# Kernel optimization log

Hardware: AMD Instinct MI355X
Metric: run time of the kernel (lower is better)

## Reference

```python
import jax, jax.numpy as jnp
import numpy as np

N_NODES = 30000
N_EDGES = 480000
N_GRAPHS = 64
NEG_SLOPE = 0.2


def gat_layer(h, src, dst, W, a_l, a_r, b):
    # h: [N, F_in], W: [F_in, H*D], a_l/a_r: [H, D], b: [H*D]
    N = h.shape[0]
    H, D = a_l.shape
    feat = (h @ W).reshape(N, H, D)
    el = jnp.sum(feat * a_l[None], axis=-1)  # [N, H]
    er = jnp.sum(feat * a_r[None], axis=-1)  # [N, H]
    e = jax.nn.leaky_relu(el[src] + er[dst], NEG_SLOPE)  # [E, H]
    # edge-softmax over incoming edges of each dst node (numerically stable)
    emax = jax.ops.segment_max(e, dst, num_segments=N)          # [N, H]
    ex = jnp.exp(e - emax[dst])                                  # [E, H]
    denom = jax.ops.segment_sum(ex, dst, num_segments=N)        # [N, H]
    alpha = ex / denom[dst]                                      # [E, H]
    msg = feat[src] * alpha[..., None]                           # [E, H, D]
    out = jax.ops.segment_sum(msg, dst, num_segments=N)         # [N, H, D]
    return out.reshape(N, H * D) + b


def setup_inputs() -> dict:
    key = jax.random.key(0)
    ks = jax.random.split(key, 16)
    feat = jax.random.normal(ks[0], (N_NODES, 6), dtype=jnp.float32)
    src = jax.random.randint(ks[1], (N_EDGES,), 0, N_NODES)
    dst = jax.random.randint(ks[2], (N_EDGES,), 0, N_NODES)
    graph_id = jnp.sort(jax.random.randint(ks[3], (N_NODES,), 0, N_GRAPHS))
    s = 0.1
    W1 = jax.random.normal(ks[4], (6, 128), dtype=jnp.float32) * s
    al1 = jax.random.normal(ks[5], (4, 32), dtype=jnp.float32) * s
    ar1 = jax.random.normal(ks[6], (4, 32), dtype=jnp.float32) * s
    b1 = jnp.zeros((128,), dtype=jnp.float32)
    W2 = jax.random.normal(ks[7], (128, 128), dtype=jnp.float32) * s
    al2 = jax.random.normal(ks[8], (4, 32), dtype=jnp.float32) * s
    ar2 = jax.random.normal(ks[9], (4, 32), dtype=jnp.float32) * s
    b2 = jnp.zeros((128,), dtype=jnp.float32)
    W3 = jax.random.normal(ks[10], (128, 256), dtype=jnp.float32) * s
    al3 = jax.random.normal(ks[11], (4, 64), dtype=jnp.float32) * s
    ar3 = jax.random.normal(ks[12], (4, 64), dtype=jnp.float32) * s
    b3 = jnp.zeros((256,), dtype=jnp.float32)
    return {"feat": feat, "src": src, "dst": dst, "graph_id": graph_id,
            "W1": W1, "al1": al1, "ar1": ar1, "b1": b1,
            "W2": W2, "al2": al2, "ar2": ar2, "b2": b2,
            "W3": W3, "al3": al3, "ar3": ar3, "b3": b3}


def reference(feat, src, dst, graph_id, W1, al1, ar1, b1, W2, al2, ar2, b2, W3, al3, ar3, b3):
    h = gat_layer(feat, src, dst, W1, al1, ar1, b1)  # [N, 128]
    h = jax.nn.relu(h)                                # dropout is identity in eval
    h = gat_layer(h, src, dst, W2, al2, ar2, b2)      # [N, 128]
    h = jax.nn.relu(h)
    h = gat_layer(h, src, dst, W3, al3, ar3, b3)      # [N, 256]
    # dgl.mean_nodes over batched graphs
    hs = jax.ops.segment_sum(h, graph_id, num_segments=N_GRAPHS)  # [G, 256]
    cnt = jax.ops.segment_sum(jnp.ones((h.shape[0],), h.dtype), graph_id, num_segments=N_GRAPHS)
    hg = hs / jnp.maximum(cnt, 1.0)[:, None]
    return hg
```

## Files before the change

kernel.cpp:

```cpp
#include <hip/hip_runtime.h>

typedef _Float16 h4 __attribute__((ext_vector_type(4)));
typedef _Float16 h8v __attribute__((ext_vector_type(8)));
typedef float f4v __attribute__((ext_vector_type(4)));
typedef float f32x8 __attribute__((ext_vector_type(8)));


__global__ void zero_i32(int* __restrict__ p, int n) {
    int i = blockIdx.x * blockDim.x + threadIdx.x;
    if (i < n) p[i] = 0;
}

__global__ void hist_kernel(const int* __restrict__ dst, int* __restrict__ counts, int E) {
    int i = blockIdx.x * blockDim.x + threadIdx.x;
    if (i < E) atomicAdd(&counts[dst[i]], 1);
}

__global__ void scan_block(const int* __restrict__ counts, int* __restrict__ rowptr,
                           int* __restrict__ bsum, int n) {
    __shared__ int wsum[16];
    const int tid = threadIdx.x;
    const int lane = tid & 63, wv = tid >> 6;
    const int i = blockIdx.x * 1024 + tid;
    int v = (i < n) ? counts[i] : 0;
    int x = v;
#pragma unroll
    for (int off = 1; off < 64; off <<= 1) {
        int t = __shfl_up(x, off);
        if (lane >= off) x += t;
    }
    if (lane == 63) wsum[wv] = x;
    __syncthreads();
    if (tid < 16) {
        int y = wsum[tid];
#pragma unroll
        for (int off = 1; off < 16; off <<= 1) {
            int t = __shfl_up(y, off);
            if (tid >= off) y += t;
        }
        wsum[tid] = y;
    }
    __syncthreads();
    int woff = (wv > 0) ? wsum[wv - 1] : 0;
    if (i < n) rowptr[i] = woff + x - v;
    if (tid == 0) bsum[blockIdx.x] = wsum[15];
}

__global__ void scan_tops(int* __restrict__ bsum, int* __restrict__ rowptr, int nb, int n) {
    const int tid = threadIdx.x;
    int v = (tid < nb) ? bsum[tid] : 0;
    int x = v;
#pragma unroll
    for (int off = 1; off < 64; off <<= 1) {
        int t = __shfl_up(x, off);
        if (tid >= off) x += t;
    }
    if (tid < nb) bsum[tid] = x - v;
    if (tid == 63) rowptr[n] = x;
}

__global__ void scan_add(int* __restrict__ rowptr, const int* __restrict__ bsum, int n) {
    int b = blockIdx.x;
    int i = b * 1024 + threadIdx.x;
    if (i < n && b > 0) rowptr[i] += bsum[b];
}

__global__ void scatter_kernel(const int* __restrict__ src, const int* __restrict__ dst,
                               const int* __restrict__ rowptr, int* __restrict__ cursor,
                               int* __restrict__ srcs, int E) {
    int i = blockIdx.x * blockDim.x + threadIdx.x;
    if (i < E) {
        int d = dst[i];
        int p = rowptr[d] + atomicAdd(&cursor[d], 1);
        srcs[p] = src[i];
    }
}

template <int K, int FOUT>
__global__ void pack_w(const float* __restrict__ W, _Float16* __restrict__ Wp) {
    constexpr int KS = K / 32;
    constexpr int CT = FOUT / 16;
    int idx = blockIdx.x * blockDim.x + threadIdx.x;
    if (idx >= CT * KS * 64) return;
    int l = idx & 63;
    int ks = (idx >> 6) % KS;
    int ct = idx / (64 * KS);
    int kbase = ks * 32 + (l >> 4) * 8;
    int col = ct * 16 + (l & 15);
    h8v v;
#pragma unroll
    for (int e = 0; e < 8; e++) v[e] = (_Float16)W[(size_t)(kbase + e) * FOUT + col];
    *reinterpret_cast<h8v*>(&Wp[(size_t)idx * 8]) = v;
}

template <int FIN, int FOUT, int D, bool RELU_IN>
__global__ void gemm_att(const float* __restrict__ A, const float* __restrict__ bin,
                         const float* __restrict__ W, const float* __restrict__ al,
                         const float* __restrict__ ar, _Float16* __restrict__ feat,
                         float* __restrict__ el, float* __restrict__ er, int N) {
    constexpr int R = 16;
    constexpr int H = FOUT / D;
    constexpr int T = FOUT / 2;
    __shared__ __align__(16) float As[FIN][R + 4];
    const int j = threadIdx.x;
    const int h0 = j / D;
    const int h1 = (j + T) / D;
    const float alv0 = al[j],     arv0 = ar[j];
    const float alv1 = al[j + T], arv1 = ar[j + T];
    const int row0 = blockIdx.x * R;

    for (int idx = threadIdx.x; idx < R * FIN; idx += T) {
        int r = idx / FIN, k = idx % FIN;
        int rr = row0 + r;
        float v = 0.f;
        if (rr < N) {
            v = A[(size_t)rr * FIN + k];
            if constexpr (RELU_IN) { v += bin[k]; v = fmaxf(v, 0.f); }
        }
        As[k][r] = v;
    }
    __syncthreads();

    float acc0[R], acc1[R];
#pragma unroll
    for (int r = 0; r < R; r++) { acc0[r] = 0.f; acc1[r] = 0.f; }

    for (int k = 0; k < FIN; k++) {
        float w0 = W[(size_t)k * FOUT + j];
        float w1 = W[(size_t)k * FOUT + j + T];
        const float4* ap = reinterpret_cast<const float4*>(&As[k][0]);
        float av[16];
        *reinterpret_cast<float4*>(&av[0])  = ap[0];
        *reinterpret_cast<float4*>(&av[4])  = ap[1];
        *reinterpret_cast<float4*>(&av[8])  = ap[2];
        *reinterpret_cast<float4*>(&av[12]) = ap[3];
#pragma unroll
        for (int r = 0; r < R; r++) {
            acc0[r] += av[r] * w0;
            acc1[r] += av[r] * w1;
        }
    }

#pragma unroll
    for (int r = 0; r < R; r++) {
        int rr = row0 + r;
        if (rr >= N) break;
        float v0 = acc0[r], v1 = acc1[r];
        feat[(size_t)rr * FOUT + j] = (_Float16)v0;
        feat[(size_t)rr * FOUT + j + T] = (_Float16)v1;
        float vl0 = v0 * alv0, vr0 = v0 * arv0;
        float vl1 = v1 * alv1, vr1 = v1 * arv1;
#pragma unroll
        for (int off = D / 2; off >= 1; off >>= 1) {
            vl0 += __shfl_xor(vl0, off);
            vr0 += __shfl_xor(vr0, off);
            vl1 += __shfl_xor(vl1, off);
            vr1 += __shfl_xor(vr1, off);
        }
        if ((j % D) == 0) {
            el[(size_t)rr * H + h0] = vl0;
            er[(size_t)rr * H + h0] = vr0;
            el[(size_t)rr * H + h1] = vl1;
            er[(size_t)rr * H + h1] = vr1;
        }
    }
}

template <int K, int FOUT, int D, bool RELU_IN>
__global__ __launch_bounds__(256)
void gemm_mfma(const float* __restrict__ A, const float* __restrict__ bin,
               const _Float16* __restrict__ Wp, const float* __restrict__ al,
               const float* __restrict__ ar, _Float16* __restrict__ feat,
               float* __restrict__ el, float* __restrict__ er, int N) {
    constexpr int RB  = 32;
    constexpr int KS  = K / 32;
    constexpr int CHW = FOUT / 2;
    constexpr int CTW = CHW / 16;
    constexpr int CTH = D / 16;
    constexpr int HW  = CTW / CTH;
    constexpr int H   = FOUT / D;
    constexpr int STR = K + 8;
    __shared__ _Float16 As[RB * STR];
    const int tid = threadIdx.x;
    const int w  = tid >> 6;
    const int l  = tid & 63;
    const int rt = w >> 1;
    const int ch = w & 1;
    const int row0 = blockIdx.x * RB;

    constexpr int NV4 = RB * K / 4;
    for (int v = tid; v < NV4; v += 256) {
        int r  = v / (K / 4);
        int kv = (v % (K / 4)) * 4;
        int rr = row0 + r;
        float4 x = {0.f, 0.f, 0.f, 0.f};
        if (rr < N) {
            x = *reinterpret_cast<const float4*>(&A[(size_t)rr * K + kv]);
            if constexpr (RELU_IN) {
                float4 bv = *reinterpret_cast<const float4*>(&bin[kv]);
                x.x = fmaxf(x.x + bv.x, 0.f);
                x.y = fmaxf(x.y + bv.y, 0.f);
                x.z = fmaxf(x.z + bv.z, 0.f);
                x.w = fmaxf(x.w + bv.w, 0.f);
            }
        }
        h4 hv;
        hv[0] = (_Float16)x.x; hv[1] = (_Float16)x.y;
        hv[2] = (_Float16)x.z; hv[3] = (_Float16)x.w;
        *reinterpret_cast<h4*>(&As[r * STR + kv]) = hv;
    }
    __syncthreads();

    h8v afrag[KS];
    {
        const _Float16* base = &As[(rt * 16 + (l & 15)) * STR + ((l >> 4) * 8)];
#pragma unroll
        for (int ks = 0; ks < KS; ks++)
            afrag[ks] = *reinterpret_cast<const h8v*>(&base[ks * 32]);
    }

    const h8v* Wv = reinterpret_cast<const h8v*>(Wp);
    const int ct0 = ch * CTW;
    f4v acc[CTW];
#pragma unroll
    for (int c = 0; c < CTW; c++) acc[c] = (f4v){0.f, 0.f, 0.f, 0.f};

    h8v bfr[2][KS];
#pragma unroll
    for (int ks = 0; ks < KS; ks++) bfr[0][ks] = Wv[(size_t)((ct0 * KS + ks) * 64 + l)];
#pragma unroll
    for (int c = 0; c < CTW; c++) {
        const int cur = c & 1, nxt = cur ^ 1;
        if (c + 1 < CTW) {
#pragma unroll
            for (int ks = 0; ks < KS; ks++)
                bfr[nxt][ks] = Wv[(size_t)(((ct0 + c + 1) * KS + ks) * 64 + l)];
        }
#pragma unroll
        for (int ks = 0; ks < KS; ks++)
            acc[c] = __builtin_amdgcn_mfma_f32_16x16x32_f16(afrag[ks], bfr[cur][ks], acc[c], 0, 0, 0);
    }

    float elp[HW][4], erp[HW][4];
#pragma unroll
    for (int hh = 0; hh < HW; hh++)
#pragma unroll
        for (int r = 0; r < 4; r++) { elp[hh][r] = 0.f; erp[hh][r] = 0.f; }

#pragma unroll
    for (int c = 0; c < CTW; c++) {
        const int col = ch * CHW + c * 16 + (l & 15);
        const float alv = al[col], arv = ar[col];
        const int hh = c / CTH;
#pragma unroll
        for (int r = 0; r < 4; r++) {
            float v = acc[c][r];
            elp[hh][r] += v * alv;
            erp[hh][r] += v * arv;
            int rr = row0 + rt * 16 + (l >> 4) * 4 + r;
            if (rr < N) feat[(size_t)rr * FOUT + col] = (_Float16)v;
        }
    }
#pragma unroll
    for (int hh = 0; hh < HW; hh++) {
#pragma unroll
        for (int r = 0; r < 4; r++) {
            float v = elp[hh][r], u = erp[hh][r];
#pragma unroll
            for (int off = 8; off >= 1; off >>= 1) {
                v += __shfl_xor(v, off);
                u += __shfl_xor(u, off);
            }
            if ((l & 15) == 0) {
                int rr = row0 + rt * 16 + (l >> 4) * 4 + r;
                if (rr < N) {
                    int hg = ch * HW + hh;
                    el[(size_t)rr * H + hg] = v;
                    er[(size_t)rr * H + hg] = u;
                }
            }
        }
    }
}

template <int HD, int D>
__global__ __launch_bounds__(256)
void agg_fused(const h8v* __restrict__ featH8, const float* __restrict__ el,
               const float* __restrict__ er, const int* __restrict__ srcs,
               const int* __restrict__ rowptr, f32x8* __restrict__ out, int N) {
    constexpr int TPN = HD / 8;
    constexpr int NPB = 256 / TPN;
    const int tid = threadIdx.x;
    const int ln = tid % TPN;
    const int node = blockIdx.x * NPB + tid / TPN;
    if (node >= N) return;
    const int h = ln / (D / 8);
    const int beg = rowptr[node], end = rowptr[node + 1];
    const float ern = er[(size_t)node * 4 + h];

    float s = 0.f;
    f32x8 a0 = {0,0,0,0,0,0,0,0}, a1 = a0;
    int i = beg;
    for (; i + 4 <= end; i += 4) {
        int u0 = srcs[i], u1 = srcs[i + 1], u2 = srcs[i + 2], u3 = srcs[i + 3];
        float x0 = el[(size_t)u0 * 4 + h] + ern; x0 = x0 > 0.f ? x0 : 0.2f * x0;
        float x1 = el[(size_t)u1 * 4 + h] + ern; x1 = x1 > 0.f ? x1 : 0.2f * x1;
        float x2 = el[(size_t)u2 * 4 + h] + ern; x2 = x2 > 0.f ? x2 : 0.2f * x2;
        float x3 = el[(size_t)u3 * 4 + h] + ern; x3 = x3 > 0.f ? x3 : 0.2f * x3;
        h8v f0 = featH8[(size_t)u0 * TPN + ln];
        h8v f1 = featH8[(size_t)u1 * TPN + ln];
        h8v f2 = featH8[(size_t)u2 * TPN + ln];
        h8v f3 = featH8[(size_t)u3 * TPN + ln];
        float w0 = __expf(x0), w1 = __expf(x1);
        float w2 = __expf(x2), w3 = __expf(x3);
        s += (w0 + w1) + (w2 + w3);
#pragma unroll
        for (int k = 0; k < 8; k++) {
            a0[k] += w0 * (float)f0[k];
            a1[k] += w1 * (float)f1[k];
            a0[k] += w2 * (float)f2[k];
            a1[k] += w3 * (float)f3[k];
        }
    }
    for (; i < end; i++) {
        int u = srcs[i];
        float x = el[(size_t)u * 4 + h] + ern; x = x > 0.f ? x : 0.2f * x;
        h8v f = featH8[(size_t)u * TPN + ln];
        float w = __expf(x);
        s += w;
#pragma unroll
        for (int k = 0; k < 8; k++) a0[k] += w * (float)f[k];
    }
    const float inv = (s > 0.f) ? 1.f / s : 0.f;
    f32x8 o;
#pragma unroll
    for (int k = 0; k < 8; k++) o[k] = (a0[k] + a1[k]) * inv;
    out[(size_t)node * TPN + ln] = o;
}


__device__ __forceinline__ int lower_bound_i(const int* __restrict__ a, int n, int key) {
    int lo = 0, hi = n;
    while (lo < hi) {
        int mid = (lo + hi) >> 1;
        if (a[mid] < key) lo = mid + 1; else hi = mid;
    }
    return lo;
}

__global__ void readout_partial(const float* __restrict__ agg, const int* __restrict__ gid,
                                float* __restrict__ part, int N, int C, int SL) {
    int g = blockIdx.x / SL, slice = blockIdx.x % SL;
    int c = threadIdx.x;
    int start = lower_bound_i(gid, N, g);
    int end = lower_bound_i(gid, N, g + 1);
    float sum = 0.f;
    for (int n = start + slice; n < end; n += SL) sum += agg[(size_t)n * C + c];
    part[((size_t)g * SL + slice) * C + c] = sum;
}

__global__ void readout_final(const float* __restrict__ part, const float* __restrict__ b3,
                              const int* __restrict__ gid, float* __restrict__ out,
                              int N, int C, int SL) {
    int g = blockIdx.x, c = threadIdx.x;
    int start = lower_bound_i(gid, N, g);
    int end = lower_bound_i(gid, N, g + 1);
    int cnt = end - start;
    float s = 0.f;
    for (int k = 0; k < SL; k++) s += part[((size_t)g * SL + k) * C + c];
    out[(size_t)g * C + c] = (cnt > 0) ? s / (float)cnt + b3[c] : 0.f;
}


extern "C" void kernel_launch(void* const* d_in, const int* in_sizes, int n_in,
                              void* d_out, int out_size, void* d_ws, size_t ws_size,
                              hipStream_t stream) {
    const float* feat0 = (const float*)d_in[0];
    const int* src = (const int*)d_in[1];
    const int* dst = (const int*)d_in[2];
    const int* gid = (const int*)d_in[3];
    const float* W1 = (const float*)d_in[4];
    const float* al1 = (const float*)d_in[5];
    const float* ar1 = (const float*)d_in[6];
    const float* b1 = (const float*)d_in[7];
    const float* W2 = (const float*)d_in[8];
    const float* al2 = (const float*)d_in[9];
    const float* ar2 = (const float*)d_in[10];
    const float* b2 = (const float*)d_in[11];
    const float* W3 = (const float*)d_in[12];
    const float* al3 = (const float*)d_in[13];
    const float* ar3 = (const float*)d_in[14];
    const float* b3 = (const float*)d_in[15];

    const int N = in_sizes[0] / 6;
    const int E = in_sizes[1];
    const int G = 64;
    const int SL = 8;
    float* out = (float*)d_out;

    char* wsp = (char*)d_ws;
    auto alloc = [&](size_t bytes) -> char* {
        char* p = wsp;
        wsp += (bytes + 255) & ~(size_t)255;
        return p;
    };
    int* counts   = (int*)alloc((size_t)N * 4);
    int* rowptr   = (int*)alloc((size_t)(N + 1) * 4);
    int* cursor   = (int*)alloc((size_t)N * 4);
    int* bsum     = (int*)alloc(64 * 4);
    int* srcs     = (int*)alloc((size_t)E * 4);
    float* el     = (float*)alloc((size_t)N * 4 * 4);
    float* er     = (float*)alloc((size_t)N * 4 * 4);
    _Float16* featH = (_Float16*)alloc((size_t)N * 256 * 2);
    float* aggB   = (float*)alloc((size_t)N * 256 * 4);
    float* part   = (float*)alloc((size_t)G * SL * 256 * 4);
    _Float16* Wp2 = (_Float16*)alloc((size_t)128 * 128 * 2);
    _Float16* Wp3 = (_Float16*)alloc((size_t)128 * 256 * 2);

    const int nb = (N + 1023) / 1024;
    const int zspan = (int)(((char*)bsum - (char*)counts) / 4) + 64;
    zero_i32<<<dim3((zspan + 255) / 256), dim3(256), 0, stream>>>(counts, zspan);
    hist_kernel<<<dim3((E + 255) / 256), dim3(256), 0, stream>>>(dst, counts, E);
    scan_block<<<dim3(nb), dim3(1024), 0, stream>>>(counts, rowptr, bsum, N);
    scan_tops<<<dim3(1), dim3(64), 0, stream>>>(bsum, rowptr, nb, N);
    scan_add<<<dim3(nb), dim3(1024), 0, stream>>>(rowptr, bsum, N);
    scatter_kernel<<<dim3((E + 255) / 256), dim3(256), 0, stream>>>(
        src, dst, rowptr, cursor, srcs, E);

    pack_w<128, 128><<<dim3(8), dim3(256), 0, stream>>>(W2, Wp2);
    pack_w<128, 256><<<dim3(16), dim3(256), 0, stream>>>(W3, Wp3);

    gemm_att<6, 128, 32, false><<<dim3((N + 15) / 16), dim3(64), 0, stream>>>(
        feat0, nullptr, W1, al1, ar1, featH, el, er, N);
    agg_fused<128, 32><<<dim3((N + 15) / 16), dim3(256), 0, stream>>>(
        (const h8v*)featH, el, er, srcs, rowptr, (f32x8*)aggB, N);

    gemm_mfma<128, 128, 32, true><<<dim3((N + 31) / 32), dim3(256), 0, stream>>>(
        aggB, b1, Wp2, al2, ar2, featH, el, er, N);
    agg_fused<128, 32><<<dim3((N + 15) / 16), dim3(256), 0, stream>>>(
        (const h8v*)featH, el, er, srcs, rowptr, (f32x8*)aggB, N);

    gemm_mfma<128, 256, 64, true><<<dim3((N + 31) / 32), dim3(256), 0, stream>>>(
        aggB, b2, Wp3, al3, ar3, featH, el, er, N);
    agg_fused<256, 64><<<dim3((N + 7) / 8), dim3(256), 0, stream>>>(
        (const h8v*)featH, el, er, srcs, rowptr, (f32x8*)aggB, N);

    readout_partial<<<dim3(G * SL), dim3(256), 0, stream>>>(aggB, gid, part, N, 256, SL);
    readout_final<<<dim3(G), dim3(256), 0, stream>>>(part, b3, gid, out, N, 256, SL);
}
```

Before: 213.5 us.

## Fuse bias+ReLU into aggregation epilogue with fp16 output, merge small launches

New measurement: 209.9 us. About the same (-1.7%).

```diff
diff --git a/kernel.cpp b/kernel.cpp
--- a/kernel.cpp
+++ b/kernel.cpp
@@ -46,23 +46,26 @@
     if (tid == 0) bsum[blockIdx.x] = wsum[15];
 }
 
-__global__ void scan_tops(int* __restrict__ bsum, int* __restrict__ rowptr, int nb, int n) {
+__global__ void scan_add_tops(int* __restrict__ rowptr, const int* __restrict__ bsum,
+                              int nb, int n) {
+    __shared__ int off_s, tot_s;
+    const int b = blockIdx.x;
     const int tid = threadIdx.x;
-    int v = (tid < nb) ? bsum[tid] : 0;
-    int x = v;
-#pragma unroll
-    for (int off = 1; off < 64; off <<= 1) {
-        int t = __shfl_up(x, off);
-        if (tid >= off) x += t;
-    }
-    if (tid < nb) bsum[tid] = x - v;
-    if (tid == 63) rowptr[n] = x;
-}
-
-__global__ void scan_add(int* __restrict__ rowptr, const int* __restrict__ bsum, int n) {
-    int b = blockIdx.x;
-    int i = b * 1024 + threadIdx.x;
-    if (i < n && b > 0) rowptr[i] += bsum[b];
+    if (tid < 64) {
+        int v = (tid < nb) ? bsum[tid] : 0;
+        int x = v;
+#pragma unroll
+        for (int off = 1; off < 64; off <<= 1) {
+            int t = __shfl_up(x, off);
+            if (tid >= off) x += t;
+        }
+        if (tid == 63) tot_s = x;
+        if (tid == b) off_s = x - v;
+    }
+    __syncthreads();
+    int i = b * 1024 + tid;
+    if (i < n) rowptr[i] += off_s;
+    if (b == 0 && tid == 0) rowptr[n] = tot_s;
 }
 
 __global__ void scatter_kernel(const int* __restrict__ src, const int* __restrict__ dst,
@@ -76,15 +79,19 @@
     }
 }
 
-template <int K, int FOUT>
-__global__ void pack_w(const float* __restrict__ W, _Float16* __restrict__ Wp) {
-    constexpr int KS = K / 32;
-    constexpr int CT = FOUT / 16;
+__global__ void pack_w_both(const float* __restrict__ W2, _Float16* __restrict__ Wp2,
+                            const float* __restrict__ W3, _Float16* __restrict__ Wp3) {
     int idx = blockIdx.x * blockDim.x + threadIdx.x;
-    if (idx >= CT * KS * 64) return;
+    const float* W; _Float16* Wp; int FOUT;
+    if (idx < 2048) { W = W2; Wp = Wp2; FOUT = 128; }
+    else {
+        idx -= 2048;
+        if (idx >= 4096) return;
+        W = W3; Wp = Wp3; FOUT = 256;
+    }
     int l = idx & 63;
-    int ks = (idx >> 6) % KS;
-    int ct = idx / (64 * KS);
+    int ks = (idx >> 6) & 3;
+    int ct = idx >> 8;
     int kbase = ks * 32 + (l >> 4) * 8;
     int col = ct * 16 + (l & 15);
     h8v v;
@@ -93,11 +100,11 @@
     *reinterpret_cast<h8v*>(&Wp[(size_t)idx * 8]) = v;
 }
 
-template <int FIN, int FOUT, int D, bool RELU_IN>
-__global__ void gemm_att(const float* __restrict__ A, const float* __restrict__ bin,
-                         const float* __restrict__ W, const float* __restrict__ al,
-                         const float* __restrict__ ar, _Float16* __restrict__ feat,
-                         float* __restrict__ el, float* __restrict__ er, int N) {
+template <int FIN, int FOUT, int D>
+__global__ void gemm_att(const float* __restrict__ A, const float* __restrict__ W,
+                         const float* __restrict__ al, const float* __restrict__ ar,
+                         _Float16* __restrict__ feat, float* __restrict__ el,
+                         float* __restrict__ er, int N) {
     constexpr int R = 16;
     constexpr int H = FOUT / D;
     constexpr int T = FOUT / 2;
@@ -112,12 +119,7 @@
     for (int idx = threadIdx.x; idx < R * FIN; idx += T) {
         int r = idx / FIN, k = idx % FIN;
         int rr = row0 + r;
-        float v = 0.f;
-        if (rr < N) {
-            v = A[(size_t)rr * FIN + k];
-            if constexpr (RELU_IN) { v += bin[k]; v = fmaxf(v, 0.f); }
-        }
-        As[k][r] = v;
+        As[k][r] = (rr < N) ? A[(size_t)rr * FIN + k] : 0.f;
     }
     __syncthreads();
 
@@ -166,12 +168,12 @@
     }
 }
 
-template <int K, int FOUT, int D, bool RELU_IN>
+template <int K, int FOUT, int D>
 __global__ __launch_bounds__(256)
-void gemm_mfma(const float* __restrict__ A, const float* __restrict__ bin,
-               const _Float16* __restrict__ Wp, const float* __restrict__ al,
-               const float* __restrict__ ar, _Float16* __restrict__ feat,
-               float* __restrict__ el, float* __restrict__ er, int N) {
+void gemm_mfma(const _Float16* __restrict__ A, const _Float16* __restrict__ Wp,
+               const float* __restrict__ al, const float* __restrict__ ar,
+               _Float16* __restrict__ feat, float* __restrict__ el,
+               float* __restrict__ er, int N) {
     constexpr int RB  = 32;
     constexpr int KS  = K / 32;
     constexpr int CHW = FOUT / 2;
@@ -188,26 +190,14 @@
     const int ch = w & 1;
     const int row0 = blockIdx.x * RB;
 
-    constexpr int NV4 = RB * K / 4;
-    for (int v = tid; v < NV4; v += 256) {
-        int r  = v / (K / 4);
-        int kv = (v % (K / 4)) * 4;
+    constexpr int NV8 = RB * K / 8;
+    for (int v = tid; v < NV8; v += 256) {
+        int r  = v / (K / 8);
+        int kv = (v % (K / 8)) * 8;
         int rr = row0 + r;
-        float4 x = {0.f, 0.f, 0.f, 0.f};
-        if (rr < N) {
-            x = *reinterpret_cast<const float4*>(&A[(size_t)rr * K + kv]);
-            if constexpr (RELU_IN) {
-                float4 bv = *reinterpret_cast<const float4*>(&bin[kv]);
-                x.x = fmaxf(x.x + bv.x, 0.f);
-                x.y = fmaxf(x.y + bv.y, 0.f);
-                x.z = fmaxf(x.z + bv.z, 0.f);
-                x.w = fmaxf(x.w + bv.w, 0.f);
-            }
-        }
-        h4 hv;
-        hv[0] = (_Float16)x.x; hv[1] = (_Float16)x.y;
-        hv[2] = (_Float16)x.z; hv[3] = (_Float16)x.w;
-        *reinterpret_cast<h4*>(&As[r * STR + kv]) = hv;
+        h8v x = {};
+        if (rr < N) x = *reinterpret_cast<const h8v*>(&A[(size_t)rr * K + kv]);
+        *reinterpret_cast<h8v*>(&As[r * STR + kv]) = x;
     }
     __syncthreads();
 
@@ -283,11 +273,12 @@
     }
 }
 
-template <int HD, int D>
+template <int HD, int D, bool FP16OUT>
 __global__ __launch_bounds__(256)
 void agg_fused(const h8v* __restrict__ featH8, const float* __restrict__ el,
                const float* __restrict__ er, const int* __restrict__ srcs,
-               const int* __restrict__ rowptr, f32x8* __restrict__ out, int N) {
+               const int* __restrict__ rowptr, const float* __restrict__ bias,
+               void* __restrict__ outp, int N) {
     constexpr int TPN = HD / 8;
     constexpr int NPB = 256 / TPN;
     const int tid = threadIdx.x;
@@ -300,17 +291,29 @@
 
     float s = 0.f;
     f32x8 a0 = {0,0,0,0,0,0,0,0}, a1 = a0;
+
     int i = beg;
+    int alend = (beg + 3) & ~3;
+    if (alend > end) alend = end;
+    for (; i < alend; i++) {
+        int u = srcs[i];
+        float x = el[(size_t)u * 4 + h] + ern; x = x > 0.f ? x : 0.2f * x;
+        h8v f = featH8[(size_t)u * TPN + ln];
+        float w = __expf(x);
+        s += w;
+#pragma unroll
+        for (int k = 0; k < 8; k++) a0[k] += w * (float)f[k];
+    }
     for (; i + 4 <= end; i += 4) {
-        int u0 = srcs[i], u1 = srcs[i + 1], u2 = srcs[i + 2], u3 = srcs[i + 3];
-        float x0 = el[(size_t)u0 * 4 + h] + ern; x0 = x0 > 0.f ? x0 : 0.2f * x0;
-        float x1 = el[(size_t)u1 * 4 + h] + ern; x1 = x1 > 0.f ? x1 : 0.2f * x1;
-        float x2 = el[(size_t)u2 * 4 + h] + ern; x2 = x2 > 0.f ? x2 : 0.2f * x2;
-        float x3 = el[(size_t)u3 * 4 + h] + ern; x3 = x3 > 0.f ? x3 : 0.2f * x3;
-        h8v f0 = featH8[(size_t)u0 * TPN + ln];
-        h8v f1 = featH8[(size_t)u1 * TPN + ln];
-        h8v f2 = featH8[(size_t)u2 * TPN + ln];
-        h8v f3 = featH8[(size_t)u3 * TPN + ln];
+        int4 uu = *reinterpret_cast<const int4*>(&srcs[i]);
+        float x0 = el[(size_t)uu.x * 4 + h] + ern; x0 = x0 > 0.f ? x0 : 0.2f * x0;
+        float x1 = el[(size_t)uu.y * 4 + h] + ern; x1 = x1 > 0.f ? x1 : 0.2f * x1;
+        float x2 = el[(size_t)uu.z * 4 + h] + ern; x2 = x2 > 0.f ? x2 : 0.2f * x2;
+        float x3 = el[(size_t)uu.w * 4 + h] + ern; x3 = x3 > 0.f ? x3 : 0.2f * x3;
+        h8v f0 = featH8[(size_t)uu.x * TPN + ln];
+        h8v f1 = featH8[(size_t)uu.y * TPN + ln];
+        h8v f2 = featH8[(size_t)uu.z * TPN + ln];
+        h8v f3 = featH8[(size_t)uu.w * TPN + ln];
         float w0 = __expf(x0), w1 = __expf(x1);
         float w2 = __expf(x2), w3 = __expf(x3);
         s += (w0 + w1) + (w2 + w3);
@@ -332,10 +335,21 @@
         for (int k = 0; k < 8; k++) a0[k] += w * (float)f[k];
     }
     const float inv = (s > 0.f) ? 1.f / s : 0.f;
-    f32x8 o;
-#pragma unroll
-    for (int k = 0; k < 8; k++) o[k] = (a0[k] + a1[k]) * inv;
-    out[(size_t)node * TPN + ln] = o;
+    if constexpr (FP16OUT) {
+        const float4 b0 = *reinterpret_cast<const float4*>(&bias[ln * 8]);
+        const float4 b1v = *reinterpret_cast<const float4*>(&bias[ln * 8 + 4]);
+        float bb[8] = {b0.x, b0.y, b0.z, b0.w, b1v.x, b1v.y, b1v.z, b1v.w};
+        h8v o;
+#pragma unroll
+        for (int k = 0; k < 8; k++)
+            o[k] = (_Float16)fmaxf((a0[k] + a1[k]) * inv + bb[k], 0.f);
+        reinterpret_cast<h8v*>(outp)[(size_t)node * TPN + ln] = o;
+    } else {
+        f32x8 o;
+#pragma unroll
+        for (int k = 0; k < 8; k++) o[k] = (a0[k] + a1[k]) * inv;
+        reinterpret_cast<f32x8*>(outp)[(size_t)node * TPN + ln] = o;
+    }
 }
 
 
@@ -412,6 +426,7 @@
     float* el     = (float*)alloc((size_t)N * 4 * 4);
     float* er     = (float*)alloc((size_t)N * 4 * 4);
     _Float16* featH = (_Float16*)alloc((size_t)N * 256 * 2);
+    _Float16* aggH  = (_Float16*)alloc((size_t)N * 128 * 2);
     float* aggB   = (float*)alloc((size_t)N * 256 * 4);
     float* part   = (float*)alloc((size_t)G * SL * 256 * 4);
     _Float16* Wp2 = (_Float16*)alloc((size_t)128 * 128 * 2);
@@ -422,28 +437,26 @@
     zero_i32<<<dim3((zspan + 255) / 256), dim3(256), 0, stream>>>(counts, zspan);
     hist_kernel<<<dim3((E + 255) / 256), dim3(256), 0, stream>>>(dst, counts, E);
     scan_block<<<dim3(nb), dim3(1024), 0, stream>>>(counts, rowptr, bsum, N);
-    scan_tops<<<dim3(1), dim3(64), 0, stream>>>(bsum, rowptr, nb, N);
-    scan_add<<<dim3(nb), dim3(1024), 0, stream>>>(rowptr, bsum, N);
+    scan_add_tops<<<dim3(nb), dim3(1024), 0, stream>>>(rowptr, bsum, nb, N);
     scatter_kernel<<<dim3((E + 255) / 256), dim3(256), 0, stream>>>(
         src, dst, rowptr, cursor, srcs, E);
 
-    pack_w<128, 128><<<dim3(8), dim3(256), 0, stream>>>(W2, Wp2);
-    pack_w<128, 256><<<dim3(16), dim3(256), 0, stream>>>(W3, Wp3);
-
-    gemm_att<6, 128, 32, false><<<dim3((N + 15) / 16), dim3(64), 0, stream>>>(
-        feat0, nullptr, W1, al1, ar1, featH, el, er, N);
-    agg_fused<128, 32><<<dim3((N + 15) / 16), dim3(256), 0, stream>>>(
-        (const h8v*)featH, el, er, srcs, rowptr, (f32x8*)aggB, N);
-
-    gemm_mfma<128, 128, 32, true><<<dim3((N + 31) / 32), dim3(256), 0, stream>>>(
-        aggB, b1, Wp2, al2, ar2, featH, el, er, N);
-    agg_fused<128, 32><<<dim3((N + 15) / 16), dim3(256), 0, stream>>>(
-        (const h8v*)featH, el, er, srcs, rowptr, (f32x8*)aggB, N);
-
-    gemm_mfma<128, 256, 64, true><<<dim3((N + 31) / 32), dim3(256), 0, stream>>>(
-        aggB, b2, Wp3, al3, ar3, featH, el, er, N);
-    agg_fused<256, 64><<<dim3((N + 7) / 8), dim3(256), 0, stream>>>(
-        (const h8v*)featH, el, er, srcs, rowptr, (f32x8*)aggB, N);
+    pack_w_both<<<dim3(24), dim3(256), 0, stream>>>(W2, Wp2, W3, Wp3);
+
+    gemm_att<6, 128, 32><<<dim3((N + 15) / 16), dim3(64), 0, stream>>>(
+        feat0, W1, al1, ar1, featH, el, er, N);
+    agg_fused<128, 32, true><<<dim3((N + 15) / 16), dim3(256), 0, stream>>>(
+        (const h8v*)featH, el, er, srcs, rowptr, b1, aggH, N);
+
+    gemm_mfma<128, 128, 32><<<dim3((N + 31) / 32), dim3(256), 0, stream>>>(
+        aggH, Wp2, al2, ar2, featH, el, er, N);
+    agg_fused<128, 32, true><<<dim3((N + 15) / 16), dim3(256), 0, stream>>>(
+        (const h8v*)featH, el, er, srcs, rowptr, b2, aggH, N);
+
+    gemm_mfma<128, 256, 64><<<dim3((N + 31) / 32), dim3(256), 0, stream>>>(
+        aggH, Wp3, al3, ar3, featH, el, er, N);
+    agg_fused<256, 64, false><<<dim3((N + 7) / 8), dim3(256), 0, stream>>>(
+        (const h8v*)featH, el, er, srcs, rowptr, nullptr, aggB, N);
 
     readout_partial<<<dim3(G * SL), dim3(256), 0, stream>>>(aggB, gid, part, N, 256, SL);
     readout_final<<<dim3(G), dim3(256), 0, stream>>>(part, b3, gid, out, N, 256, SL);
```
